# Performance work log

Measured on AMD Instinct MI355X. Metric: run time of the kernel, lower is better.

## Reference

```python
import jax, jax.numpy as jnp
import numpy as np

N, DIN, DOUT = 8192, 256, 64
SLOPE = 0.2  # leakyrelu negative slope
NEG_INF = -9e15


def _leaky(z):
    return jnp.where(z >= 0, z, SLOPE * z)


def setup_inputs() -> dict:
    key = jax.random.key(0)
    k1, k2, k3, k4 = jax.random.split(key, 4)
    x = jax.random.normal(k1, (N, DIN), dtype=jnp.float32)
    w = jax.random.normal(k2, (DIN, DOUT), dtype=jnp.float32) * 0.1
    a = jax.random.normal(k3, (2 * DOUT, 1), dtype=jnp.float32) * 0.1
    adj = (jax.random.uniform(k4, (N, N)) < 0.05).astype(jnp.float32)
    adj = jnp.maximum(adj, jnp.eye(N, dtype=jnp.float32))
    ones1 = jnp.ones((1,), dtype=jnp.float32)
    return {
        "x": x, "adj": adj, "w": w, "a": a,
        "a_coeff": ones1, "b_coeff": ones1 * 0.5,
        "c_coeff": ones1, "d_coeff": ones1 * 0.1,
    }


def reference(x, adj, w, a, a_coeff, b_coeff, c_coeff, d_coeff):
    h = x @ w  # [N, DOUT]
    # a_input[i,j] = concat(h_i, h_j); a_input @ a == (h @ a1)_i + (h @ a2)_j
    a1, a2 = a[:DOUT, 0], a[DOUT:, 0]
    e_raw = (h @ a1)[:, None] + (h @ a2)[None, :]  # [N, N]
    e = _leaky(c_coeff * e_raw + d_coeff)
    adj_transformed = a_coeff * adj + b_coeff
    e_transformed = _leaky(adj_transformed) * e
    attention = jax.nn.softmax(jnp.where(adj > 0, e_transformed, NEG_INF), axis=1)
    # dropout=0.0 (eval) -> identity
    h_prime = attention @ h  # [N, DOUT]
    return jax.nn.elu(h_prime)  # concat=True
```

## Files before the change

kernel.cpp:

```cpp
#include <hip/hip_runtime.h>
#include <hip/hip_bf16.h>
#include <math.h>

#define NN 8192
#define DINK 256
#define DOUTK 64
#define SLOPEF 0.2f
#define LOG2E 1.442695040888963f
#define CHUNKS 4
#define CHCOLS (NN / CHUNKS)
#define NRG (NN / 16)
#define TW 128
#define TSTRIDE 129
#define NITER (CHCOLS / TW)

typedef __attribute__((ext_vector_type(8))) short short8;
typedef __attribute__((ext_vector_type(4))) float f32x4;

__device__ float g_h[NN * DOUTK];
__device__ unsigned short g_hbT[DOUTK * NN];
__device__ float g_s1[NN];
__device__ float g_s2[NN];
__device__ float4 g_coef;
__device__ float g_pm[NRG * CHUNKS * 16];
__device__ float g_pd[NRG * CHUNKS * 16];
__device__ float g_pacc[NRG * CHUNKS * 16 * DOUTK];

struct PtrPack { const float* p[8]; int n; };

__device__ __forceinline__ short f2bf(float x) {
  __hip_bfloat16 h = __float2bfloat16(x);
  return *reinterpret_cast<short*>(&h);
}

__global__ void classify_kernel(PtrPack pk) {
  if (threadIdx.x != 0 || blockIdx.x != 0) return;
  float vals[8];
  const int n = pk.n;
  for (int i = 0; i < n && i < 8; ++i) vals[i] = pk.p[i][0];
  float bc = 0.f, dc = 0.f, onev[2] = {1.f, 1.f};
  int nb = 0, nd = 0, ones = 0;
  for (int i = 0; i < n && i < 8; ++i) {
    const float v = vals[i];
    if (fabsf(v - 0.5f) < 0.05f)      { bc = v; ++nb; }
    else if (fabsf(v - 0.1f) < 0.05f) { dc = v; ++nd; }
    else if (fabsf(v - 1.0f) < 0.05f && ones < 2) onev[ones++] = v;
  }
  if (nb == 1 && nd == 1 && ones == 2) g_coef = make_float4(onev[0], bc, onev[1], dc);
  else if (n >= 4) g_coef = make_float4(vals[0], vals[1], vals[2], vals[3]);
  else g_coef = make_float4(1.f, 0.5f, 1.f, 0.1f);
}

__global__ __launch_bounds__(256) void prep_kernel(
    const float* __restrict__ x, const float* __restrict__ w,
    const float* __restrict__ a) {
  __shared__ float wl[DINK * DOUTK];
  for (int idx = threadIdx.x; idx < DINK * DOUTK; idx += 256) wl[idx] = w[idx];
  __syncthreads();

  const int lane = threadIdx.x & 63;
  const int wave = threadIdx.x >> 6;
  const float a1 = a[lane];
  const float a2 = a[DOUTK + lane];
  const float4 cf = g_coef;

  for (int r = 0; r < 4; ++r) {
    const int row = blockIdx.x * 16 + wave * 4 + r;
    const float4* xr = (const float4*)(x + (size_t)row * DINK);
    float acc = 0.f;
#pragma unroll 8
    for (int k4 = 0; k4 < DINK / 4; ++k4) {
      const float4 xv = xr[k4];
      acc = fmaf(xv.x, wl[(k4 * 4 + 0) * DOUTK + lane], acc);
      acc = fmaf(xv.y, wl[(k4 * 4 + 1) * DOUTK + lane], acc);
      acc = fmaf(xv.z, wl[(k4 * 4 + 2) * DOUTK + lane], acc);
      acc = fmaf(xv.w, wl[(k4 * 4 + 3) * DOUTK + lane], acc);
    }
    g_h[row * DOUTK + lane] = acc;
    float p1 = acc * a1, p2 = acc * a2;
#pragma unroll
    for (int off = 32; off; off >>= 1) {
      p1 += __shfl_xor(p1, off);
      p2 += __shfl_xor(p2, off);
    }
    if (lane == 0) {
      g_s1[row] = fmaf(cf.z, p1, cf.w) * LOG2E;
      g_s2[row] = cf.z * p2 * LOG2E;
    }
  }
}

__global__ __launch_bounds__(256) void transpose_kernel() {
  __shared__ float t[64][65];
  const int tid = threadIdx.x;
  const int jb = blockIdx.x * 64;
  const int d = tid & 63, j4 = tid >> 6;
#pragma unroll
  for (int i = 0; i < 16; ++i) {
    const int jj = i * 4 + j4;
    t[jj][d] = g_h[(size_t)(jb + jj) * DOUTK + d];
  }
  __syncthreads();
  const int jj2 = tid & 63, d4 = tid >> 6;
#pragma unroll
  for (int i = 0; i < 16; ++i) {
    const int dd_ = i * 4 + d4;
    const int j = jb + jj2;
    g_hbT[(size_t)(j >> 5) * 2048 + dd_ * 32 + (j & 31)] = (unsigned short)f2bf(t[jj2][dd_]);
  }
}

__global__ __launch_bounds__(256) void attn_kernel(
    const float* __restrict__ adj) {
  const int tid = threadIdx.x;
  const int lane = tid & 63;
  const int w = tid >> 6;
  const int ln = lane & 15;
  const int g = lane >> 4;
  const int rowgroup = blockIdx.x >> 2;
  const int chunk = blockIdx.x & 3;
  const int rowbase = rowgroup * 16;
  const int row = rowbase + ln;

  __shared__ float smem[4288];
  float* abuf = smem;
  float* lacc = smem;
  float* mmb = smem + 4160;
  float* ddb = smem + 4224;

  const float4 cf = g_coef;
  const float ltz = cf.x + cf.y;
  const float ltc = fmaxf(ltz, SLOPEF * ltz);
  const float base2 = g_s1[row];
  const float4* s2v4 = (const float4*)g_s2;
  const unsigned short* hb = g_hbT;

  f32x4 acc0 = {0.f, 0.f, 0.f, 0.f}, acc1 = acc0, acc2 = acc0, acc3 = acc0;
  float m_run = -1.0e30f;
  float den = 0.f;

  const int srow = 4 * w + (lane >> 5);
  const int scol = (lane & 31) * 4;
  const size_t adj_base = (size_t)(rowbase + srow) * NN + chunk * CHCOLS + scol;

  float4 p0, p1;
  p0 = *(const float4*)(adj + adj_base);
  p1 = *(const float4*)(adj + adj_base + 2 * NN);
  {
    float* b0 = abuf + srow * TSTRIDE + scol;
    b0[0] = p0.x; b0[1] = p0.y; b0[2] = p0.z; b0[3] = p0.w;
    float* b1 = abuf + (srow + 2) * TSTRIDE + scol;
    b1[0] = p1.x; b1[1] = p1.y; b1[2] = p1.z; b1[3] = p1.w;
  }
  __syncthreads();

  for (int it = 0; it < NITER; ++it) {
    if (it + 1 < NITER) {
      p0 = *(const float4*)(adj + adj_base + (size_t)(it + 1) * TW);
      p1 = *(const float4*)(adj + adj_base + (size_t)(it + 1) * TW + 2 * NN);
    }

    const int jb = chunk * CHCOLS + it * TW + w * 32;
    const unsigned short* hp = hb + (size_t)(jb >> 5) * 2048 + ln * 32 + g * 8;
    const short8 b0 = *(const short8*)(hp + 0 * 512);
    const short8 b1 = *(const short8*)(hp + 1 * 512);
    const short8 b2 = *(const short8*)(hp + 2 * 512);
    const short8 b3 = *(const short8*)(hp + 3 * 512);
    const float4 t0 = s2v4[(jb + g * 8) >> 2];
    const float4 t1 = s2v4[((jb + g * 8) >> 2) + 1];
    const float te[8] = {t0.x, t0.y, t0.z, t0.w, t1.x, t1.y, t1.z, t1.w};

    const float* tb = abuf + (it & 1) * 2064 + ln * TSTRIDE + w * 32 + g * 8;
    float v[8];
    float vmax = -3.0e38f;
#pragma unroll
    for (int i = 0; i < 8; ++i) {
      const float ez = base2 + te[i];
      const float e2 = fmaxf(ez, SLOPEF * ez);
      const float vv = ltc * e2;
      v[i] = tb[i] > 0.f ? vv : -3.0e38f;
      vmax = fmaxf(vmax, v[i]);
    }

    if (__any(vmax > m_run)) {
      float rowmax = fmaxf(vmax, __shfl_xor(vmax, 16));
      rowmax = fmaxf(rowmax, __shfl_xor(rowmax, 32));
      const float mnew = fmaxf(m_run, rowmax);
      const float r = exp2f(m_run - mnew);
      den *= r;
      const float r0 = __shfl(r, g * 4 + 0);
      const float r1 = __shfl(r, g * 4 + 1);
      const float r2 = __shfl(r, g * 4 + 2);
      const float r3 = __shfl(r, g * 4 + 3);
      acc0[0] *= r0; acc0[1] *= r1; acc0[2] *= r2; acc0[3] *= r3;
      acc1[0] *= r0; acc1[1] *= r1; acc1[2] *= r2; acc1[3] *= r3;
      acc2[0] *= r0; acc2[1] *= r1; acc2[2] *= r2; acc2[3] *= r3;
      acc3[0] *= r0; acc3[1] *= r1; acc3[2] *= r2; acc3[3] *= r3;
      m_run = mnew;
    }

    short8 af;
#pragma unroll
    for (int i = 0; i < 8; ++i) {
      const float p = exp2f(v[i] - m_run);
      den += p;
      af[i] = f2bf(p);
    }
    acc0 = __builtin_amdgcn_mfma_f32_16x16x32_bf16(af, b0, acc0, 0, 0, 0);
    acc1 = __builtin_amdgcn_mfma_f32_16x16x32_bf16(af, b1, acc1, 0, 0, 0);
    acc2 = __builtin_amdgcn_mfma_f32_16x16x32_bf16(af, b2, acc2, 0, 0, 0);
    acc3 = __builtin_amdgcn_mfma_f32_16x16x32_bf16(af, b3, acc3, 0, 0, 0);

    if (it + 1 < NITER) {
      float* b0w = abuf + ((it + 1) & 1) * 2064 + srow * TSTRIDE + scol;
      b0w[0] = p0.x; b0w[1] = p0.y; b0w[2] = p0.z; b0w[3] = p0.w;
      float* b1w = abuf + ((it + 1) & 1) * 2064 + (srow + 2) * TSTRIDE + scol;
      b1w[0] = p1.x; b1w[1] = p1.y; b1w[2] = p1.z; b1w[3] = p1.w;
    }
    __syncthreads();
  }

  den += __shfl_xor(den, 16);
  den += __shfl_xor(den, 32);
  if (lane < 16) { mmb[w * 16 + ln] = m_run; ddb[w * 16 + ln] = den; }
#pragma unroll
  for (int reg = 0; reg < 4; ++reg) {
    const int cr = g * 4 + reg;
    lacc[(w * 16 + cr) * 65 + 0 * 16 + ln] = acc0[reg];
    lacc[(w * 16 + cr) * 65 + 1 * 16 + ln] = acc1[reg];
    lacc[(w * 16 + cr) * 65 + 2 * 16 + ln] = acc2[reg];
    lacc[(w * 16 + cr) * 65 + 3 * 16 + ln] = acc3[reg];
  }
  __syncthreads();

  const int pg = rowgroup * CHUNKS + chunk;
#pragma unroll
  for (int k = 0; k < 4; ++k) {
    const int p = tid + 256 * k;
    const int r = p >> 6, d = p & 63;
    const float m0 = mmb[0 * 16 + r], m1 = mmb[1 * 16 + r];
    const float m2 = mmb[2 * 16 + r], m3 = mmb[3 * 16 + r];
    const float ms = fmaxf(fmaxf(m0, m1), fmaxf(m2, m3));
    const float e0 = exp2f(m0 - ms), e1 = exp2f(m1 - ms);
    const float e2 = exp2f(m2 - ms), e3 = exp2f(m3 - ms);
    const float dn = ddb[0 * 16 + r] * e0 + ddb[1 * 16 + r] * e1 +
                     ddb[2 * 16 + r] * e2 + ddb[3 * 16 + r] * e3;
    const float nm = lacc[(0 * 16 + r) * 65 + d] * e0 + lacc[(1 * 16 + r) * 65 + d] * e1 +
                     lacc[(2 * 16 + r) * 65 + d] * e2 + lacc[(3 * 16 + r) * 65 + d] * e3;
    if (d == 0) { g_pm[pg * 16 + r] = ms; g_pd[pg * 16 + r] = dn; }
    g_pacc[(size_t)(pg * 16 + r) * DOUTK + d] = nm;
  }
}

__global__ __launch_bounds__(256) void merge_kernel(float* __restrict__ out) {
  const int rowgroup = blockIdx.x;
  const int tid = threadIdx.x;
#pragma unroll
  for (int k = 0; k < 4; ++k) {
    const int p = tid + 256 * k;
    const int r = p >> 6, d = p & 63;
    float mA[CHUNKS], ms = -3.0e38f;
#pragma unroll
    for (int c = 0; c < CHUNKS; ++c) {
      mA[c] = g_pm[(rowgroup * CHUNKS + c) * 16 + r];
      ms = fmaxf(ms, mA[c]);
    }
    float dn = 0.f, nm = 0.f;
#pragma unroll
    for (int c = 0; c < CHUNKS; ++c) {
      const float e = exp2f(mA[c] - ms);
      dn = fmaf(g_pd[(rowgroup * CHUNKS + c) * 16 + r], e, dn);
      nm = fmaf(g_pacc[(size_t)((rowgroup * CHUNKS + c) * 16 + r) * DOUTK + d], e, nm);
    }
    const float hp = nm / dn;
    out[(size_t)(rowgroup * 16 + r) * DOUTK + d] = hp > 0.f ? hp : expm1f(hp);
  }
}

extern "C" void kernel_launch(void* const* d_in, const int* in_sizes, int n_in,
                              void* d_out, int out_size, void* d_ws, size_t ws_size,
                              hipStream_t stream) {
  const float *x = nullptr, *adj = nullptr, *w = nullptr, *a = nullptr;
  PtrPack pk; pk.n = 0;
  for (int i = 0; i < n_in; ++i) {
    switch (in_sizes[i]) {
      case NN * DINK:    x = (const float*)d_in[i]; break;
      case NN * NN:      adj = (const float*)d_in[i]; break;
      case DINK * DOUTK: w = (const float*)d_in[i]; break;
      case 2 * DOUTK:    a = (const float*)d_in[i]; break;
      case 1: if (pk.n < 8) pk.p[pk.n++] = (const float*)d_in[i]; break;
      default: break;
    }
  }
  if (!x)   x   = (const float*)d_in[0];
  if (!adj) adj = (const float*)d_in[1];
  if (!w)   w   = (const float*)d_in[2];
  if (!a)   a   = (const float*)d_in[3];
  if (pk.n == 0) {
    pk.p[0] = (const float*)d_in[4]; pk.p[1] = (const float*)d_in[5];
    pk.p[2] = (const float*)d_in[6]; pk.p[3] = (const float*)d_in[7];
    pk.n = 4;
  }

  float* out = (float*)d_out;

  classify_kernel<<<1, 64, 0, stream>>>(pk);
  prep_kernel<<<NN / 16, 256, 0, stream>>>(x, w, a);
  transpose_kernel<<<NN / 64, 256, 0, stream>>>();
  attn_kernel<<<NRG * CHUNKS, 256, 0, stream>>>(adj);
  merge_kernel<<<NRG, 256, 0, stream>>>(out);
}
```

Before: 103.9 us.

## Fold classify and transpose into prep kernel, vectorize adjacency LDS traffic

Removes the single-thread classify kernel and the transpose kernel. Each consumer now classifies the coefficients inline, and prep writes the bf16 transposed h tile straight from shared memory, so the fp32 g_h round trip through global memory goes away. Prep now runs 32 rows per 512-thread block. In the attention kernel the LDS row stride is padded to 132 so adjacency tiles can be written and read with float4 accesses instead of scalar ones. This cuts launch count and LDS instruction count, at the cost of redundant coefficient classification in every block and possible bank conflicts from the new stride.

```diff
diff --git a/kernel.cpp b/kernel.cpp
--- a/kernel.cpp
+++ b/kernel.cpp
@@ -11,17 +11,16 @@
 #define CHCOLS (NN / CHUNKS)
 #define NRG (NN / 16)
 #define TW 128
-#define TSTRIDE 129
+#define TSTRIDE 132
 #define NITER (CHCOLS / TW)
 
 typedef __attribute__((ext_vector_type(8))) short short8;
+typedef __attribute__((ext_vector_type(4))) short short4v;
 typedef __attribute__((ext_vector_type(4))) float f32x4;
 
-__device__ float g_h[NN * DOUTK];
 __device__ unsigned short g_hbT[DOUTK * NN];
 __device__ float g_s1[NN];
 __device__ float g_s2[NN];
-__device__ float4 g_coef;
 __device__ float g_pm[NRG * CHUNKS * 16];
 __device__ float g_pd[NRG * CHUNKS * 16];
 __device__ float g_pacc[NRG * CHUNKS * 16 * DOUTK];
@@ -33,39 +32,40 @@
   return *reinterpret_cast<short*>(&h);
 }
 
-__global__ void classify_kernel(PtrPack pk) {
-  if (threadIdx.x != 0 || blockIdx.x != 0) return;
+__device__ __forceinline__ float4 classify_dev(const PtrPack& pk) {
   float vals[8];
-  const int n = pk.n;
-  for (int i = 0; i < n && i < 8; ++i) vals[i] = pk.p[i][0];
+  const int n = pk.n < 8 ? pk.n : 8;
+  for (int i = 0; i < n; ++i) vals[i] = pk.p[i][0];
   float bc = 0.f, dc = 0.f, onev[2] = {1.f, 1.f};
   int nb = 0, nd = 0, ones = 0;
-  for (int i = 0; i < n && i < 8; ++i) {
+  for (int i = 0; i < n; ++i) {
     const float v = vals[i];
     if (fabsf(v - 0.5f) < 0.05f)      { bc = v; ++nb; }
     else if (fabsf(v - 0.1f) < 0.05f) { dc = v; ++nd; }
     else if (fabsf(v - 1.0f) < 0.05f && ones < 2) onev[ones++] = v;
   }
-  if (nb == 1 && nd == 1 && ones == 2) g_coef = make_float4(onev[0], bc, onev[1], dc);
-  else if (n >= 4) g_coef = make_float4(vals[0], vals[1], vals[2], vals[3]);
-  else g_coef = make_float4(1.f, 0.5f, 1.f, 0.1f);
-}
-
-__global__ __launch_bounds__(256) void prep_kernel(
+  if (nb == 1 && nd == 1 && ones == 2) return make_float4(onev[0], bc, onev[1], dc);
+  if (n >= 4) return make_float4(vals[0], vals[1], vals[2], vals[3]);
+  return make_float4(1.f, 0.5f, 1.f, 0.1f);
+}
+
+__global__ __launch_bounds__(512) void prep_kernel(
     const float* __restrict__ x, const float* __restrict__ w,
-    const float* __restrict__ a) {
+    const float* __restrict__ a, PtrPack pk) {
   __shared__ float wl[DINK * DOUTK];
-  for (int idx = threadIdx.x; idx < DINK * DOUTK; idx += 256) wl[idx] = w[idx];
+  __shared__ float h32[32][65];
+  const float4 cf = classify_dev(pk);
+  for (int idx = threadIdx.x; idx < DINK * DOUTK; idx += 512) wl[idx] = w[idx];
   __syncthreads();
 
   const int lane = threadIdx.x & 63;
   const int wave = threadIdx.x >> 6;
   const float a1 = a[lane];
   const float a2 = a[DOUTK + lane];
-  const float4 cf = g_coef;
 
   for (int r = 0; r < 4; ++r) {
-    const int row = blockIdx.x * 16 + wave * 4 + r;
+    const int jl = wave * 4 + r;
+    const int row = blockIdx.x * 32 + jl;
     const float4* xr = (const float4*)(x + (size_t)row * DINK);
     float acc = 0.f;
 #pragma unroll 8
@@ -76,7 +76,7 @@
       acc = fmaf(xv.z, wl[(k4 * 4 + 2) * DOUTK + lane], acc);
       acc = fmaf(xv.w, wl[(k4 * 4 + 3) * DOUTK + lane], acc);
     }
-    g_h[row * DOUTK + lane] = acc;
+    h32[jl][lane] = acc;
     float p1 = acc * a1, p2 = acc * a2;
 #pragma unroll
     for (int off = 32; off; off >>= 1) {
@@ -88,30 +88,21 @@
       g_s2[row] = cf.z * p2 * LOG2E;
     }
   }
-}
-
-__global__ __launch_bounds__(256) void transpose_kernel() {
-  __shared__ float t[64][65];
-  const int tid = threadIdx.x;
-  const int jb = blockIdx.x * 64;
-  const int d = tid & 63, j4 = tid >> 6;
-#pragma unroll
-  for (int i = 0; i < 16; ++i) {
-    const int jj = i * 4 + j4;
-    t[jj][d] = g_h[(size_t)(jb + jj) * DOUTK + d];
-  }
-  __syncthreads();
-  const int jj2 = tid & 63, d4 = tid >> 6;
-#pragma unroll
-  for (int i = 0; i < 16; ++i) {
-    const int dd_ = i * 4 + d4;
-    const int j = jb + jj2;
-    g_hbT[(size_t)(j >> 5) * 2048 + dd_ * 32 + (j & 31)] = (unsigned short)f2bf(t[jj2][dd_]);
-  }
+  __syncthreads();
+
+  unsigned short* dst = g_hbT + (size_t)blockIdx.x * 2048;
+  const int t4 = threadIdx.x * 4;
+  short4v v;
+#pragma unroll
+  for (int i = 0; i < 4; ++i) {
+    const int idx = t4 + i;
+    v[i] = f2bf(h32[idx & 31][idx >> 5]);
+  }
+  *(short4v*)(dst + t4) = v;
 }
 
 __global__ __launch_bounds__(256) void attn_kernel(
-    const float* __restrict__ adj) {
+    const float* __restrict__ adj, PtrPack pk) {
   const int tid = threadIdx.x;
   const int lane = tid & 63;
   const int w = tid >> 6;
@@ -128,7 +119,7 @@
   float* mmb = smem + 4160;
   float* ddb = smem + 4224;
 
-  const float4 cf = g_coef;
+  const float4 cf = classify_dev(pk);
   const float ltz = cf.x + cf.y;
   const float ltc = fmaxf(ltz, SLOPEF * ltz);
   const float base2 = g_s1[row];
@@ -146,12 +137,8 @@
   float4 p0, p1;
   p0 = *(const float4*)(adj + adj_base);
   p1 = *(const float4*)(adj + adj_base + 2 * NN);
-  {
-    float* b0 = abuf + srow * TSTRIDE + scol;
-    b0[0] = p0.x; b0[1] = p0.y; b0[2] = p0.z; b0[3] = p0.w;
-    float* b1 = abuf + (srow + 2) * TSTRIDE + scol;
-    b1[0] = p1.x; b1[1] = p1.y; b1[2] = p1.z; b1[3] = p1.w;
-  }
+  *(float4*)(abuf + srow * TSTRIDE + scol) = p0;
+  *(float4*)(abuf + (srow + 2) * TSTRIDE + scol) = p1;
   __syncthreads();
 
   for (int it = 0; it < NITER; ++it) {
@@ -170,7 +157,11 @@
     const float4 t1 = s2v4[((jb + g * 8) >> 2) + 1];
     const float te[8] = {t0.x, t0.y, t0.z, t0.w, t1.x, t1.y, t1.z, t1.w};
 
-    const float* tb = abuf + (it & 1) * 2064 + ln * TSTRIDE + w * 32 + g * 8;
+    const float* tb = abuf + (it & 1) * 2112 + ln * TSTRIDE + w * 32 + g * 8;
+    const float4 A = *(const float4*)tb;
+    const float4 B = *(const float4*)(tb + 4);
+    const float ae[8] = {A.x, A.y, A.z, A.w, B.x, B.y, B.z, B.w};
+
     float v[8];
     float vmax = -3.0e38f;
 #pragma unroll
@@ -178,7 +169,7 @@
       const float ez = base2 + te[i];
       const float e2 = fmaxf(ez, SLOPEF * ez);
       const float vv = ltc * e2;
-      v[i] = tb[i] > 0.f ? vv : -3.0e38f;
+      v[i] = ae[i] > 0.f ? vv : -3.0e38f;
       vmax = fmaxf(vmax, v[i]);
     }
 
@@ -212,10 +203,8 @@
     acc3 = __builtin_amdgcn_mfma_f32_16x16x32_bf16(af, b3, acc3, 0, 0, 0);
 
     if (it + 1 < NITER) {
-      float* b0w = abuf + ((it + 1) & 1) * 2064 + srow * TSTRIDE + scol;
-      b0w[0] = p0.x; b0w[1] = p0.y; b0w[2] = p0.z; b0w[3] = p0.w;
-      float* b1w = abuf + ((it + 1) & 1) * 2064 + (srow + 2) * TSTRIDE + scol;
-      b1w[0] = p1.x; b1w[1] = p1.y; b1w[2] = p1.z; b1w[3] = p1.w;
+      *(float4*)(abuf + ((it + 1) & 1) * 2112 + srow * TSTRIDE + scol) = p0;
+      *(float4*)(abuf + ((it + 1) & 1) * 2112 + (srow + 2) * TSTRIDE + scol) = p1;
     }
     __syncthreads();
   }
@@ -304,9 +293,7 @@
 
   float* out = (float*)d_out;
 
-  classify_kernel<<<1, 64, 0, stream>>>(pk);
-  prep_kernel<<<NN / 16, 256, 0, stream>>>(x, w, a);
-  transpose_kernel<<<NN / 64, 256, 0, stream>>>();
-  attn_kernel<<<NRG * CHUNKS, 256, 0, stream>>>(adj);
+  prep_kernel<<<NN / 32, 512, 0, stream>>>(x, w, a, pk);
+  attn_kernel<<<NRG * CHUNKS, 256, 0, stream>>>(adj, pk);
   merge_kernel<<<NRG, 256, 0, stream>>>(out);
 }
```

Result: no change. 102.1 us (-1.8%).
